# Kernel optimization log

Hardware: AMD Instinct MI355X
Metric: run time of the kernel (lower is better)

## Reference

```python
import jax, jax.numpy as jnp
import numpy as np

TOPK = 5    # top-k nearest neighbours for the loss
TOPKP = 10  # top-k' for the constraint mask


def _normalize(x):
    # matches torch F.normalize(dim=1) for well-conditioned random inputs
    return x / jnp.linalg.norm(x, axis=1, keepdims=True)


def setup_inputs() -> dict:
    key = jax.random.key(0)
    ks = jax.random.split(key, 9)
    B, D, K, N = 256, 512, 128000, 100000
    queue = _normalize(jax.random.normal(ks[2], (K, D), jnp.float32))  # init normalizes queue
    return {
        "query": jax.random.normal(ks[0], (B, D), jnp.float32),
        "current_target": jax.random.normal(ks[1], (B, D), jnp.float32),
        "queue": queue,
        "pool": jax.random.normal(ks[3], (2, N, D), jnp.float32),
        "labels_bank": jax.random.randint(ks[4], (B * 0 + K,), 0, 1000, dtype=jnp.int32).astype(jnp.int64) if False else jax.random.randint(ks[4], (K,), 0, 1000),
        "index_queue": jax.random.randint(ks[5], (K,), 0, N),
        "pool_qindex": jax.random.randint(ks[6], (N,), 0, 2),
        "labels": jax.random.randint(ks[7], (B,), 0, 1000),
        "indices": jax.random.randint(ks[8], (B,), 0, N),
    }


def reference(query, current_target, queue, pool, labels_bank, index_queue,
              pool_qindex, labels, indices):
    B = query.shape[0]
    q = _normalize(query)                                   # [B, D]
    # target branch is under torch.no_grad(); queue/pool are detached buffers
    t = jax.lax.stop_gradient(_normalize(current_target))   # [B, D]
    queue = jax.lax.stop_gradient(queue)
    pool = jax.lax.stop_gradient(pool)

    # --- _dequeue_and_enqueue with queue_ptr = 0 ---
    pool = pool.at[pool_qindex[indices], indices].set(t)
    pool_qindex = pool_qindex.at[indices].set((pool_qindex[indices] + 1) % 2)
    queue = queue.at[:B].set(t)
    labels_bank = labels_bank.at[:B].set(labels)
    index_queue = index_queue.at[:B].set(indices)

    # --- cdist (squared L2 of unit vectors) against the 128k bank ---
    dist_t = 2.0 - 2.0 * jnp.einsum('bc,kc->bk', t, queue)  # [B, K]
    dist_q = 2.0 - 2.0 * jnp.einsum('bc,kc->bk', q, queue)  # [B, K]

    # unconstrained NN: smallest distances == largest -dist
    _, un_idx = jax.lax.top_k(-dist_t, TOPK)                # [B, TOPK]
    nn_q_un = jnp.take_along_axis(dist_q, un_idx, axis=1)

    # --- constraint branch on the epoch pool ---
    targets_prime = pool[pool_qindex[index_queue], index_queue]  # [K, D]
    ct_prime = pool[pool_qindex[indices], indices]               # [B, D]
    dist_tp = 2.0 - 2.0 * jnp.einsum('bc,kc->bk', ct_prime, targets_prime)
    _, idx_p = jax.lax.top_k(-dist_tp, TOPKP)                    # [B, TOPKP]

    # scatter -5 at constrained positions (topk indices are unique, so add == set)
    dist_t = dist_t.at[jnp.arange(B)[:, None], idx_p].add(-5.0)

    _, con_idx = jax.lax.top_k(-dist_t, TOPK)
    nn_q_con = jnp.take_along_axis(dist_q, con_idx, axis=1)

    loss = ((nn_q_con.sum(axis=1) / TOPK).mean()
            + (nn_q_un.sum(axis=1) / TOPK).mean()) / 2.0

    matches = (labels_bank[un_idx] == labels[:, None]).astype(jnp.float32)
    purity = (matches.sum(axis=1) / TOPK).mean()
    return loss, purity
```

## Files before the change

### kernel.cpp

```cpp
#include <hip/hip_runtime.h>
#include <math.h>

#define B_SZ 256
#define D_SZ 512
#define K_SZ 128000
#define N_SZ 100000

#define OFF_T     0UL
#define OFF_Q     524288UL
#define OFF_TH    1048576UL
#define OFF_CTH   1310720UL
#define OFF_NPQ   1572864UL
#define OFF_TPROW 1973248UL
#define OFF_UN    2485248UL
#define OFF_IDXP  2490880UL
#define OFF_SC    2501632UL

typedef __attribute__((ext_vector_type(4))) float    f32x4;
typedef __attribute__((ext_vector_type(8))) _Float16 f16x8;

__device__ __forceinline__ float block_sum(float v, float* red) {
  #pragma unroll
  for (int o = 32; o > 0; o >>= 1) v += __shfl_down(v, o, 64);
  const int w = threadIdx.x >> 6;
  const int l = threadIdx.x & 63;
  __syncthreads();
  if (l == 0) red[w] = v;
  __syncthreads();
  return red[0] + red[1] + red[2] + red[3];
}

__global__ __launch_bounds__(256) void prep_rows_kernel(
    const float* __restrict__ query, const float* __restrict__ ctar,
    const float* __restrict__ pool, const int* __restrict__ pool_qindex,
    const int* __restrict__ indices,
    float* __restrict__ t_f32, float* __restrict__ q_f32,
    _Float16* __restrict__ t_f16, _Float16* __restrict__ ct_f16)
{
  __shared__ float red[4];
  const int b = blockIdx.x, tid = threadIdx.x;
  const long base = (long)b * D_SZ;
  float x0 = query[base + tid], x1 = query[base + 256 + tid];
  float y0 = ctar[base + tid],  y1 = ctar[base + 256 + tid];
  float sq = block_sum(x0 * x0 + x1 * x1, red);
  float st = block_sum(y0 * y0 + y1 * y1, red);
  float rq = 1.f / sqrtf(sq);
  float rt = 1.f / sqrtf(st);
  q_f32[base + tid] = x0 * rq; q_f32[base + 256 + tid] = x1 * rq;
  float t0 = y0 * rt, t1 = y1 * rt;
  t_f32[base + tid] = t0; t_f32[base + 256 + tid] = t1;
  t_f16[base + tid] = (_Float16)t0; t_f16[base + 256 + tid] = (_Float16)t1;
  int i = indices[b];
  int slot = 1 - pool_qindex[i];
  const float* pr = pool + ((long)slot * N_SZ + i) * D_SZ;
  ct_f16[base + tid] = (_Float16)pr[tid];
  ct_f16[base + 256 + tid] = (_Float16)pr[tid + 256];
}

__global__ void prep_newpq_kernel(const int* __restrict__ pq, int* __restrict__ new_pq) {
  int i = blockIdx.x * 256 + threadIdx.x;
  if (i < N_SZ) new_pq[i] = pq[i];
}

__global__ void prep_flip_kernel(const int* __restrict__ pq, const int* __restrict__ indices,
                                 int* __restrict__ new_pq) {
  int i = indices[threadIdx.x];
  new_pq[i] = 1 - pq[i];
}

__global__ void prep_tprow_kernel(const int* __restrict__ new_pq,
                                  const int* __restrict__ index_queue,
                                  const int* __restrict__ indices,
                                  int* __restrict__ tp_row) {
  int k = blockIdx.x * 256 + threadIdx.x;
  int i = (k < B_SZ) ? indices[k] : index_queue[k];
  tp_row[k] = new_pq[i] * N_SZ + i;
}

template<int MODE>
__global__ __launch_bounds__(256) void gemm_kernel(
    const float* __restrict__ queue, const float* __restrict__ pool,
    const float* __restrict__ t_f32, const _Float16* __restrict__ A_f16,
    const int* __restrict__ tp_row, float* __restrict__ scores)
{
  __shared__ __align__(16) _Float16 B_lds[64 * 72];
  const int tid  = threadIdx.x;
  const int lane = tid & 63;
  const int w    = tid >> 6;
  const int quad = lane >> 4;
  const int l15  = lane & 15;
  const long col0 = (long)blockIdx.x * 64;

  const int brow = tid >> 2;
  const int bch  = tid & 3;
  const long gcol = col0 + brow;
  const float* bsrc;
  if (MODE == 0) {
    bsrc = (gcol < B_SZ) ? (t_f32 + gcol * D_SZ) : (queue + gcol * D_SZ);
  } else {
    bsrc = pool + (long)tp_row[gcol] * D_SZ;
  }
  bsrc += bch * 16;

  f32x4 acc[4][4];
  #pragma unroll
  for (int mt = 0; mt < 4; ++mt)
    #pragma unroll
    for (int nt = 0; nt < 4; ++nt) acc[mt][nt] = (f32x4){0.f, 0.f, 0.f, 0.f};

  const _Float16* arow = A_f16 + (long)(w * 64 + l15) * D_SZ + quad * 8;

  #pragma unroll 1
  for (int kc = 0; kc < D_SZ; kc += 64) {
    float4 f0 = *(const float4*)(bsrc + kc + 0);
    float4 f1 = *(const float4*)(bsrc + kc + 4);
    float4 f2 = *(const float4*)(bsrc + kc + 8);
    float4 f3 = *(const float4*)(bsrc + kc + 12);
    f16x8 w0, w1;
    w0[0] = (_Float16)f0.x; w0[1] = (_Float16)f0.y; w0[2] = (_Float16)f0.z; w0[3] = (_Float16)f0.w;
    w0[4] = (_Float16)f1.x; w0[5] = (_Float16)f1.y; w0[6] = (_Float16)f1.z; w0[7] = (_Float16)f1.w;
    w1[0] = (_Float16)f2.x; w1[1] = (_Float16)f2.y; w1[2] = (_Float16)f2.z; w1[3] = (_Float16)f2.w;
    w1[4] = (_Float16)f3.x; w1[5] = (_Float16)f3.y; w1[6] = (_Float16)f3.z; w1[7] = (_Float16)f3.w;
    *(f16x8*)(&B_lds[brow * 72 + bch * 16])     = w0;
    *(f16x8*)(&B_lds[brow * 72 + bch * 16 + 8]) = w1;
    __syncthreads();
    #pragma unroll
    for (int ks = 0; ks < 2; ++ks) {
      f16x8 af[4], bfr[4];
      #pragma unroll
      for (int mt = 0; mt < 4; ++mt)
        af[mt] = *(const f16x8*)(arow + (long)mt * 16 * D_SZ + kc + ks * 32);
      #pragma unroll
      for (int nt = 0; nt < 4; ++nt)
        bfr[nt] = *(const f16x8*)(&B_lds[(nt * 16 + l15) * 72 + ks * 32 + quad * 8]);
      #pragma unroll
      for (int mt = 0; mt < 4; ++mt)
        #pragma unroll
        for (int nt = 0; nt < 4; ++nt)
          acc[mt][nt] = __builtin_amdgcn_mfma_f32_16x16x32_f16(af[mt], bfr[nt], acc[mt][nt], 0, 0, 0);
    }
    __syncthreads();
  }

  #pragma unroll
  for (int mt = 0; mt < 4; ++mt) {
    int row0 = w * 64 + mt * 16 + quad * 4;
    #pragma unroll
    for (int i = 0; i < 4; ++i) {
      long rbase = (long)(row0 + i) * K_SZ + col0;
      #pragma unroll
      for (int nt = 0; nt < 4; ++nt)
        scores[rbase + nt * 16 + l15] = acc[mt][nt][i];
    }
  }
}

template<int KS>
__global__ __launch_bounds__(256) void topk_kernel(
    const float* __restrict__ scores, int* __restrict__ out_idx)
{
  __shared__ float sv[256 * KS];
  __shared__ int   si[256 * KS];
  const int r = blockIdx.x;
  const int tid = threadIdx.x;
  float bv[KS]; int bi[KS];
  #pragma unroll
  for (int j = 0; j < KS; ++j) { bv[j] = -3.4e38f; bi[j] = 0x7fffffff; }
  const float4* srow = (const float4*)(scores + (long)r * K_SZ);
  for (int it = 0; it < K_SZ / 1024; ++it) {
    float4 v4 = srow[it * 256 + tid];
    int kb = (it * 256 + tid) * 4;
    float vv[4] = {v4.x, v4.y, v4.z, v4.w};
    #pragma unroll
    for (int j = 0; j < 4; ++j) {
      float v = vv[j];
      if (v > bv[KS - 1]) {
        bv[KS - 1] = v; bi[KS - 1] = kb + j;
        #pragma unroll
        for (int m = KS - 1; m > 0; --m) {
          if (bv[m] > bv[m - 1]) {
            float tv = bv[m]; bv[m] = bv[m - 1]; bv[m - 1] = tv;
            int   ti = bi[m]; bi[m] = bi[m - 1]; bi[m - 1] = ti;
          }
        }
      }
    }
  }
  #pragma unroll
  for (int j = 0; j < KS; ++j) { sv[tid * KS + j] = bv[j]; si[tid * KS + j] = bi[j]; }
  for (int s = 128; s > 0; s >>= 1) {
    __syncthreads();
    if (tid < s) {
      int pa = tid * KS, pb = (tid + s) * KS;
      float mv[KS]; int mi[KS];
      int ia = 0, ib = 0;
      #pragma unroll
      for (int j = 0; j < KS; ++j) {
        float va = sv[pa + ia], vb = sv[pb + ib];
        int   xa = si[pa + ia], xb = si[pb + ib];
        bool ta = (va > vb) || (va == vb && xa < xb);
        mv[j] = ta ? va : vb; mi[j] = ta ? xa : xb;
        if (ta) ++ia; else ++ib;
      }
      #pragma unroll
      for (int j = 0; j < KS; ++j) { sv[pa + j] = mv[j]; si[pa + j] = mi[j]; }
    }
  }
  __syncthreads();
  if (tid < KS) out_idx[r * KS + tid] = si[tid];
}

__global__ __launch_bounds__(256) void finalize_kernel(
    const float* __restrict__ t_f32, const float* __restrict__ q_f32,
    const float* __restrict__ queue,
    const int* __restrict__ un_idx, const int* __restrict__ idxp,
    const int* __restrict__ labels_bank, const int* __restrict__ labels,
    float* __restrict__ out)
{
  __shared__ float red[4];
  __shared__ float dvals[10];
  __shared__ int   csel[5];
  const int b = blockIdx.x;
  const int tid = threadIdx.x;
  const float* trow = t_f32 + (long)b * D_SZ;
  const float* qrow = q_f32 + (long)b * D_SZ;

  #pragma unroll 1
  for (int j = 0; j < 10; ++j) {
    int c = idxp[b * 10 + j];
    const float* cp = (c < B_SZ) ? (t_f32 + (long)c * D_SZ) : (queue + (long)c * D_SZ);
    float p = trow[tid] * cp[tid] + trow[tid + 256] * cp[tid + 256];
    float s = block_sum(p, red);
    if (tid == 0) dvals[j] = 2.f - 2.f * s;
  }
  __syncthreads();
  if (tid == 0) {
    unsigned used = 0;
    for (int m = 0; m < 5; ++m) {
      int best = -1; float bd = 0.f; int bc = 0;
      for (int j = 0; j < 10; ++j) {
        if (used & (1u << j)) continue;
        float dj = dvals[j]; int cj = idxp[b * 10 + j];
        if (best < 0 || dj < bd || (dj == bd && cj < bc)) { best = j; bd = dj; bc = cj; }
      }
      used |= 1u << best;
      csel[m] = idxp[b * 10 + best];
    }
  }
  __syncthreads();

  float con_s = 0.f, un_s = 0.f;
  #pragma unroll 1
  for (int m = 0; m < 5; ++m) {
    int c = csel[m];
    const float* cp = (c < B_SZ) ? (t_f32 + (long)c * D_SZ) : (queue + (long)c * D_SZ);
    float p = qrow[tid] * cp[tid] + qrow[tid + 256] * cp[tid + 256];
    con_s += block_sum(p, red);
  }
  int match = 0;
  #pragma unroll 1
  for (int m = 0; m < 5; ++m) {
    int c = un_idx[b * 5 + m];
    const float* cp = (c < B_SZ) ? (t_f32 + (long)c * D_SZ) : (queue + (long)c * D_SZ);
    float p = qrow[tid] * cp[tid] + qrow[tid + 256] * cp[tid + 256];
    un_s += block_sum(p, red);
    if (tid == 0) {
      int lb = (c < B_SZ) ? labels[c] : labels_bank[c];
      match += (lb == labels[b]) ? 1 : 0;
    }
  }
  if (tid == 0) {
    float con_sum = 10.f - 2.f * con_s;
    float un_sum  = 10.f - 2.f * un_s;
    float lossc = (con_sum * 0.2f + un_sum * 0.2f) * 0.5f * (1.f / 256.f);
    atomicAdd(out + 0, lossc);
    atomicAdd(out + 1, (float)match * 0.2f * (1.f / 256.f));
  }
}

extern "C" void kernel_launch(void* const* d_in, const int* in_sizes, int n_in,
                              void* d_out, int out_size, void* d_ws, size_t ws_size,
                              hipStream_t stream) {
  const float* query       = (const float*)d_in[0];
  const float* ctar        = (const float*)d_in[1];
  const float* queue       = (const float*)d_in[2];
  const float* pool        = (const float*)d_in[3];
  const int*   labels_bank = (const int*)d_in[4];
  const int*   index_queue = (const int*)d_in[5];
  const int*   pool_qindex = (const int*)d_in[6];
  const int*   labels      = (const int*)d_in[7];
  const int*   indices     = (const int*)d_in[8];

  char* ws = (char*)d_ws;
  float*     t_f32  = (float*)(ws + OFF_T);
  float*     q_f32  = (float*)(ws + OFF_Q);
  _Float16*  t_f16  = (_Float16*)(ws + OFF_TH);
  _Float16*  ct_f16 = (_Float16*)(ws + OFF_CTH);
  int*       new_pq = (int*)(ws + OFF_NPQ);
  int*       tp_row = (int*)(ws + OFF_TPROW);
  int*       un_idx = (int*)(ws + OFF_UN);
  int*       idxp   = (int*)(ws + OFF_IDXP);
  float*     scores = (float*)(ws + OFF_SC);
  float*     out    = (float*)d_out;

  hipMemsetAsync(out, 0, 2 * sizeof(float), stream);

  prep_rows_kernel<<<B_SZ, 256, 0, stream>>>(query, ctar, pool, pool_qindex, indices,
                                             t_f32, q_f32, t_f16, ct_f16);
  prep_newpq_kernel<<<(N_SZ + 255) / 256, 256, 0, stream>>>(pool_qindex, new_pq);
  prep_flip_kernel<<<1, 256, 0, stream>>>(pool_qindex, indices, new_pq);
  prep_tprow_kernel<<<K_SZ / 256, 256, 0, stream>>>(new_pq, index_queue, indices, tp_row);

  gemm_kernel<0><<<K_SZ / 64, 256, 0, stream>>>(queue, pool, t_f32, t_f16, tp_row, scores);
  topk_kernel<5><<<B_SZ, 256, 0, stream>>>(scores, un_idx);

  gemm_kernel<1><<<K_SZ / 64, 256, 0, stream>>>(queue, pool, t_f32, ct_f16, tp_row, scores);
  topk_kernel<10><<<B_SZ, 256, 0, stream>>>(scores, idxp);

  finalize_kernel<<<B_SZ, 256, 0, stream>>>(t_f32, q_f32, queue, un_idx, idxp,
                                            labels_bank, labels, out);
}
```

Before: 1.045 ms.

## Fuse per-tile top-k into GEMM epilogue and merge candidates in second pass

```diff
diff --git a/kernel.cpp b/kernel.cpp
--- a/kernel.cpp
+++ b/kernel.cpp
@@ -5,6 +5,7 @@
 #define D_SZ 512
 #define K_SZ 128000
 #define N_SZ 100000
+#define NBLK (K_SZ / 64)
 
 #define OFF_T     0UL
 #define OFF_Q     524288UL
@@ -77,13 +78,16 @@
   tp_row[k] = new_pq[i] * N_SZ + i;
 }
 
-template<int MODE>
-__global__ __launch_bounds__(256) void gemm_kernel(
+template<int MODE, int KS>
+__global__ __launch_bounds__(256) void gemm_topk_kernel(
     const float* __restrict__ queue, const float* __restrict__ pool,
     const float* __restrict__ t_f32, const _Float16* __restrict__ A_f16,
-    const int* __restrict__ tp_row, float* __restrict__ scores)
+    const int* __restrict__ tp_row, unsigned long long* __restrict__ cand)
 {
-  __shared__ __align__(16) _Float16 B_lds[64 * 72];
+  __shared__ __align__(16) char smem[32 * 257 * 4];
+  _Float16* B_lds = (_Float16*)smem;
+  float*    sc    = (float*)smem;
+
   const int tid  = threadIdx.x;
   const int lane = tid & 63;
   const int w    = tid >> 6;
@@ -110,12 +114,13 @@
 
   const _Float16* arow = A_f16 + (long)(w * 64 + l15) * D_SZ + quad * 8;
 
+  float4 f0 = *(const float4*)(bsrc + 0);
+  float4 f1 = *(const float4*)(bsrc + 4);
+  float4 f2 = *(const float4*)(bsrc + 8);
+  float4 f3 = *(const float4*)(bsrc + 12);
+
   #pragma unroll 1
   for (int kc = 0; kc < D_SZ; kc += 64) {
-    float4 f0 = *(const float4*)(bsrc + kc + 0);
-    float4 f1 = *(const float4*)(bsrc + kc + 4);
-    float4 f2 = *(const float4*)(bsrc + kc + 8);
-    float4 f3 = *(const float4*)(bsrc + kc + 12);
     f16x8 w0, w1;
     w0[0] = (_Float16)f0.x; w0[1] = (_Float16)f0.y; w0[2] = (_Float16)f0.z; w0[3] = (_Float16)f0.w;
     w0[4] = (_Float16)f1.x; w0[5] = (_Float16)f1.y; w0[6] = (_Float16)f1.z; w0[7] = (_Float16)f1.w;
@@ -124,6 +129,12 @@
     *(f16x8*)(&B_lds[brow * 72 + bch * 16])     = w0;
     *(f16x8*)(&B_lds[brow * 72 + bch * 16 + 8]) = w1;
     __syncthreads();
+    if (kc + 64 < D_SZ) {
+      f0 = *(const float4*)(bsrc + kc + 64);
+      f1 = *(const float4*)(bsrc + kc + 68);
+      f2 = *(const float4*)(bsrc + kc + 72);
+      f3 = *(const float4*)(bsrc + kc + 76);
+    }
     #pragma unroll
     for (int ks = 0; ks < 2; ++ks) {
       f16x8 af[4], bfr[4];
@@ -142,46 +153,78 @@
     __syncthreads();
   }
 
-  #pragma unroll
-  for (int mt = 0; mt < 4; ++mt) {
-    int row0 = w * 64 + mt * 16 + quad * 4;
+  float bv[KS]; int bi[KS];
+  #pragma unroll
+  for (int j = 0; j < KS; ++j) { bv[j] = -3.4e38f; bi[j] = 0x7fffffff; }
+  const int row = tid;
+  #pragma unroll 1
+  for (int ch = 0; ch < 2; ++ch) {
+    __syncthreads();
     #pragma unroll
-    for (int i = 0; i < 4; ++i) {
-      long rbase = (long)(row0 + i) * K_SZ + col0;
-      #pragma unroll
-      for (int nt = 0; nt < 4; ++nt)
-        scores[rbase + nt * 16 + l15] = acc[mt][nt][i];
-    }
-  }
+    for (int mt = 0; mt < 4; ++mt) {
+      int r0 = w * 64 + mt * 16 + quad * 4;
+      #pragma unroll
+      for (int nt2 = 0; nt2 < 2; ++nt2) {
+        int lc = nt2 * 16 + l15;
+        #pragma unroll
+        for (int i = 0; i < 4; ++i)
+          sc[lc * 257 + r0 + i] = acc[mt][ch * 2 + nt2][i];
+      }
+    }
+    __syncthreads();
+    int cbase = (int)col0 + ch * 32;
+    #pragma unroll 1
+    for (int c8 = 0; c8 < 32; c8 += 8) {
+      float v[8];
+      #pragma unroll
+      for (int u = 0; u < 8; ++u) v[u] = sc[(c8 + u) * 257 + row];
+      #pragma unroll
+      for (int u = 0; u < 8; ++u) {
+        float vv = v[u];
+        if (vv > bv[KS - 1]) {
+          bv[KS - 1] = vv; bi[KS - 1] = cbase + c8 + u;
+          #pragma unroll
+          for (int m = KS - 1; m > 0; --m) {
+            if (bv[m] > bv[m - 1]) {
+              float tv = bv[m]; bv[m] = bv[m - 1]; bv[m - 1] = tv;
+              int   ti = bi[m]; bi[m] = bi[m - 1]; bi[m - 1] = ti;
+            }
+          }
+        }
+      }
+    }
+  }
+  unsigned long long* cp = cand + ((long)row * NBLK + blockIdx.x) * KS;
+  #pragma unroll
+  for (int j = 0; j < KS; ++j)
+    cp[j] = ((unsigned long long)__float_as_uint(bv[j]) << 32) | (unsigned)bi[j];
 }
 
 template<int KS>
-__global__ __launch_bounds__(256) void topk_kernel(
-    const float* __restrict__ scores, int* __restrict__ out_idx)
+__global__ __launch_bounds__(256) void merge_topk_kernel(
+    const unsigned long long* __restrict__ cand, int* __restrict__ out_idx)
 {
   __shared__ float sv[256 * KS];
   __shared__ int   si[256 * KS];
   const int r = blockIdx.x;
   const int tid = threadIdx.x;
+  const int TOT = NBLK * KS;
   float bv[KS]; int bi[KS];
   #pragma unroll
   for (int j = 0; j < KS; ++j) { bv[j] = -3.4e38f; bi[j] = 0x7fffffff; }
-  const float4* srow = (const float4*)(scores + (long)r * K_SZ);
-  for (int it = 0; it < K_SZ / 1024; ++it) {
-    float4 v4 = srow[it * 256 + tid];
-    int kb = (it * 256 + tid) * 4;
-    float vv[4] = {v4.x, v4.y, v4.z, v4.w};
-    #pragma unroll
-    for (int j = 0; j < 4; ++j) {
-      float v = vv[j];
-      if (v > bv[KS - 1]) {
-        bv[KS - 1] = v; bi[KS - 1] = kb + j;
-        #pragma unroll
-        for (int m = KS - 1; m > 0; --m) {
-          if (bv[m] > bv[m - 1]) {
-            float tv = bv[m]; bv[m] = bv[m - 1]; bv[m - 1] = tv;
-            int   ti = bi[m]; bi[m] = bi[m - 1]; bi[m - 1] = ti;
-          }
+  const unsigned long long* base = cand + (long)r * TOT;
+  #pragma unroll 1
+  for (int f = tid; f < TOT; f += 256) {
+    unsigned long long p = base[f];
+    float v = __uint_as_float((unsigned)(p >> 32));
+    int   x = (int)(unsigned)p;
+    if (v > bv[KS - 1]) {
+      bv[KS - 1] = v; bi[KS - 1] = x;
+      #pragma unroll
+      for (int m = KS - 1; m > 0; --m) {
+        if (bv[m] > bv[m - 1]) {
+          float tv = bv[m]; bv[m] = bv[m - 1]; bv[m - 1] = tv;
+          int   ti = bi[m]; bi[m] = bi[m - 1]; bi[m - 1] = ti;
         }
       }
     }
@@ -300,7 +343,7 @@
   int*       tp_row = (int*)(ws + OFF_TPROW);
   int*       un_idx = (int*)(ws + OFF_UN);
   int*       idxp   = (int*)(ws + OFF_IDXP);
-  float*     scores = (float*)(ws + OFF_SC);
+  unsigned long long* cand = (unsigned long long*)(ws + OFF_SC);
   float*     out    = (float*)d_out;
 
   hipMemsetAsync(out, 0, 2 * sizeof(float), stream);
@@ -311,11 +354,11 @@
   prep_flip_kernel<<<1, 256, 0, stream>>>(pool_qindex, indices, new_pq);
   prep_tprow_kernel<<<K_SZ / 256, 256, 0, stream>>>(new_pq, index_queue, indices, tp_row);
 
-  gemm_kernel<0><<<K_SZ / 64, 256, 0, stream>>>(queue, pool, t_f32, t_f16, tp_row, scores);
-  topk_kernel<5><<<B_SZ, 256, 0, stream>>>(scores, un_idx);
-
-  gemm_kernel<1><<<K_SZ / 64, 256, 0, stream>>>(queue, pool, t_f32, ct_f16, tp_row, scores);
-  topk_kernel<10><<<B_SZ, 256, 0, stream>>>(scores, idxp);
+  gemm_topk_kernel<0, 5><<<NBLK, 256, 0, stream>>>(queue, pool, t_f32, t_f16, tp_row, cand);
+  merge_topk_kernel<5><<<B_SZ, 256, 0, stream>>>(cand, un_idx);
+
+  gemm_topk_kernel<1, 10><<<NBLK, 256, 0, stream>>>(queue, pool, t_f32, ct_f16, tp_row, cand);
+  merge_topk_kernel<10><<<B_SZ, 256, 0, stream>>>(cand, idxp);
 
   finalize_kernel<<<B_SZ, 256, 0, stream>>>(t_f32, q_f32, queue, un_idx, idxp,
                                             labels_bank, labels, out);
```

Measured after the change: 1.257 ms. +20.3%, slower.
